# Kernel optimization log

Measured on AMD Instinct MI355X. Metric: run time of the kernel, lower is better.

The kernel has to match this reference:

```python
import jax, jax.numpy as jnp
import numpy as np

RES = 192
VOXEL_LEN = 2.0 / (RES - 1)
AABB_LO, AABB_HI = -1.0, 1.0
SH_DIM = 9
UNIFORM = 0.5

_C0 = 0.28209479177387814
_C1 = 0.4886025119029199
_C2 = (1.0925484305920792, -1.0925484305920792, 0.31539156525252005,
       -1.0925484305920792, 0.5462742152960396)

_CORNERS = np.array([[-1, -1, -1], [-1, -1, 1], [-1, 1, -1], [-1, 1, 1],
                     [1, -1, -1], [1, -1, 1], [1, 1, -1], [1, 1, 1]], dtype=np.float32)


def _sh_basis(d):
    # degree-2 real spherical harmonics basis, [B, 9]
    x, y, z = d[..., 0], d[..., 1], d[..., 2]
    return jnp.stack([
        jnp.full_like(x, _C0),
        -_C1 * y, _C1 * z, -_C1 * x,
        _C2[0] * x * y, _C2[1] * y * z,
        _C2[2] * (2.0 * z * z - x * x - y * y),
        _C2[3] * x * z, _C2[4] * (x * x - y * y),
    ], axis=-1)


def _interp_weights(xyz):
    # trilinear weights matching get_interp_weights corner ordering, [..., 8]
    x, y, z = xyz[..., 0], xyz[..., 1], xyz[..., 2]
    return jnp.stack([
        (1 - x) * (1 - y) * (1 - z), (1 - x) * (1 - y) * z,
        (1 - x) * y * (1 - z), (1 - x) * y * z,
        x * (1 - y) * (1 - z), x * (1 - y) * z,
        x * y * (1 - z), x * y * z], axis=-1)


def setup_inputs() -> dict:
    key = jax.random.key(0)
    k1, k2, k3 = jax.random.split(key, 3)
    B = 1024
    # rays originating on a radius-3 sphere, pointing roughly at the aabb center
    rays_o = jax.random.normal(k1, (B, 3), dtype=jnp.float32)
    rays_o = 3.0 * rays_o / jnp.linalg.norm(rays_o, axis=-1, keepdims=True)
    rays_d = -rays_o / 3.0 + 0.08 * jax.random.normal(k2, (B, 3), dtype=jnp.float32)
    rays_d = rays_d / jnp.linalg.norm(rays_d, axis=-1, keepdims=True)
    grid_data = 0.1 * jax.random.normal(k3, (RES ** 3, 3 * SH_DIM + 1), dtype=jnp.float32)
    grid_idx = jnp.arange(RES ** 3, dtype=jnp.int32).reshape(RES, RES, RES)
    return {"rays_o": rays_o, "rays_d": rays_d, "grid_data": grid_data,
            "grid_idx": grid_idx, "n_samples": 400}


def reference(rays_o, rays_d, grid_data, grid_idx, n_samples):
    B = rays_o.shape[0]
    step = VOXEL_LEN
    # --- get_intersections (no-grad in original) ---
    op = (AABB_HI - rays_o) / rays_d
    on = (AABB_LO - rays_o) / rays_d
    t_in = jnp.max(jnp.minimum(op, on), axis=-1)   # [B]
    t_out = jnp.min(jnp.maximum(op, on), axis=-1)  # [B]
    w = jnp.linspace(0.0, 1.0, n_samples, dtype=rays_o.dtype)
    start = t_in + UNIFORM * step
    end = t_in + UNIFORM * step * n_samples
    intrs = start[:, None] * (1.0 - w) + end[:, None] * w   # [B, S]
    intrs = jax.lax.stop_gradient(jnp.minimum(intrs, t_out[:, None]))

    # --- get_intersection_ids: neighbor voxel gather coordinates ---
    pts = rays_o[:, None, :] + intrs[:, :, None] * rays_d[:, None, :]  # [B,S,3]
    offs = jnp.asarray(_CORNERS) * (VOXEL_LEN / 2)                      # [8,3]
    neigh = pts[:, :, None, :] + offs[None, None]                       # [B,S,8,3]
    ngc = jnp.floor(neigh / VOXEL_LEN + 1e-5)
    centers = jnp.clip((ngc + 0.5) * VOXEL_LEN,
                       AABB_LO + VOXEL_LEN / 2, AABB_HI - VOXEL_LEN / 2)
    ids = jnp.clip((ngc + RES / 2).astype(jnp.int32), 0, RES - 1)
    xyzs = (pts - centers[:, :, 0, :]) / VOXEL_LEN                      # [B,S,3]
    nidx = grid_idx[ids[..., 0], ids[..., 1], ids[..., 2]]              # [B,S,8]

    # --- gather + trilinear interpolation (weights are non-diff in original) ---
    nd = grid_data[nidx]                                                 # [B,S,8,28]
    weights = jax.lax.stop_gradient(_interp_weights(xyzs))              # [B,S,8]
    feat = jnp.einsum('bsec,bse->bsc', nd, weights)                      # [B,S,28]

    sigma = feat[..., -1]                                                # [B,S]
    sh = feat[..., :-1].reshape(B, -1, 3, SH_DIM)                        # [B,S,3,9]
    dirs = rays_d / jnp.linalg.norm(rays_d, axis=-1, keepdims=True)
    rgb = jnp.einsum('bsck,bk->bsc', sh, _sh_basis(dirs))                # [B,S,3]

    # --- volumetric_rendering (uses S-1 intervals) ---
    dists = jnp.diff(intrs, axis=1) * jnp.linalg.norm(rays_d, axis=-1, keepdims=True)
    alpha = 1.0 - jnp.exp(-jax.nn.relu(sigma[:, :-1]) * dists)           # [B,S-1]
    cum = jnp.concatenate([jnp.ones((B, 1), alpha.dtype),
                           jnp.cumprod(1.0 - alpha[:, :-1] + 1e-10, axis=-1)], axis=-1)
    abs_light = alpha * cum
    acc = abs_light.sum(-1)
    rgb_map = (abs_light[..., None] * jax.nn.sigmoid(rgb[:, :-1])).sum(axis=1)  # [B,3]
    depth = jax.lax.stop_gradient((abs_light * intrs[:, :-1]).sum(-1))
    rgb_map = rgb_map + (1.0 - acc[:, None])  # white background
    return rgb_map, alpha, depth
```

## Files before the change

kernel.cpp:

```cpp
#include <hip/hip_runtime.h>
#include <cstddef>


constexpr int   RES  = 192;
constexpr float VLEN = 2.0f / 191.0f;
constexpr int   SM1  = 399;

__global__ __launch_bounds__(512) void nerf_render(
    const float* __restrict__ rays_o,
    const float* __restrict__ rays_d,
    const float* __restrict__ grid_data,
    float* __restrict__ out, int B)
{
  const int b    = blockIdx.x;
  const int tid  = threadIdx.x;
  const int wave = tid >> 6;
  const int lane = tid & 63;
  const int srel = lane >> 3;
  const int r    = lane & 7;

  __shared__ float s_alpha[SM1];
  __shared__ float s_rgb0[SM1];
  __shared__ float s_rgb1[SM1];
  __shared__ float s_rgb2[SM1];
  __shared__ float s_bs[9];

  const float ox = rays_o[b*3+0], oy = rays_o[b*3+1], oz = rays_o[b*3+2];
  const float dx = rays_d[b*3+0], dy = rays_d[b*3+1], dz = rays_d[b*3+2];

  const float opx = (1.0f - ox)/dx, onx = (-1.0f - ox)/dx;
  const float opy = (1.0f - oy)/dy, ony = (-1.0f - oy)/dy;
  const float opz = (1.0f - oz)/dz, onz = (-1.0f - oz)/dz;
  const float t_in  = fmaxf(fmaxf(fminf(opx,onx), fminf(opy,ony)), fminf(opz,onz));
  const float t_out = fminf(fminf(fmaxf(opx,onx), fmaxf(opy,ony)), fmaxf(opz,onz));
  const float h = 0.5f * VLEN;
  const float dnorm = sqrtf(dx*dx + dy*dy + dz*dz);

  {
    const float inv = 1.0f / dnorm;
    const float x = dx*inv, y = dy*inv, z = dz*inv;
    if (tid == 0) {
      s_bs[0] = 0.28209479177387814f;
      s_bs[1] = -0.4886025119029199f * y;
      s_bs[2] =  0.4886025119029199f * z;
      s_bs[3] = -0.4886025119029199f * x;
      s_bs[4] =  1.0925484305920792f * x*y;
      s_bs[5] = -1.0925484305920792f * y*z;
      s_bs[6] =  0.31539156525252005f * (2.0f*z*z - x*x - y*y);
      s_bs[7] = -1.0925484305920792f * x*z;
      s_bs[8] =  0.5462742152960396f * (x*x - y*y);
    }
  }
  __syncthreads();

  float c0[4], c1[4], c2[4], cs[4];
  #pragma unroll
  for (int j = 0; j < 4; ++j) {
    const int c = 4*r + j;
    float b0 = 0.0f, b1 = 0.0f, b2 = 0.0f, bsg = 0.0f;
    if (c < 9)       b0  = s_bs[c];
    else if (c < 18) b1  = s_bs[c - 9];
    else if (c < 27) b2  = s_bs[c - 18];
    else if (c == 27) bsg = 1.0f;
    c0[j] = b0; c1[j] = b1; c2[j] = b2; cs[j] = bsg;
  }

  float* out_rgb   = out;
  float* out_alpha = out + (size_t)B*3;
  float* out_depth = out + (size_t)B*3 + (size_t)B*SM1;

  const float hv = 0.5f * VLEN;
  const float inv_vlen = 1.0f / VLEN;

  #pragma unroll
  for (int p = 0; p < 7; ++p) {
    const int s = p*64 + wave*8 + srel;
    if (s < SM1) {
      const float t  = fminf(t_in + h*(float)(s+1), t_out);
      const float tn = fminf(t_in + h*(float)(s+2), t_out);
      const float px = ox + t*dx, py = oy + t*dy, pz = oz + t*dz;

      const float nx0 = floorf((px - hv)*inv_vlen + 1e-5f);
      const float nx1 = floorf((px + hv)*inv_vlen + 1e-5f);
      const float ny0 = floorf((py - hv)*inv_vlen + 1e-5f);
      const float ny1 = floorf((py + hv)*inv_vlen + 1e-5f);
      const float nz0 = floorf((pz - hv)*inv_vlen + 1e-5f);
      const float nz1 = floorf((pz + hv)*inv_vlen + 1e-5f);

      const int ix0 = min(max((int)(nx0 + 96.0f), 0), RES-1);
      const int ix1 = min(max((int)(nx1 + 96.0f), 0), RES-1);
      const int iy0 = min(max((int)(ny0 + 96.0f), 0), RES-1);
      const int iy1 = min(max((int)(ny1 + 96.0f), 0), RES-1);
      const int iz0 = min(max((int)(nz0 + 96.0f), 0), RES-1);
      const int iz1 = min(max((int)(nz1 + 96.0f), 0), RES-1);

      const float cx = fminf(fmaxf((nx0 + 0.5f)*VLEN, -1.0f + hv), 1.0f - hv);
      const float cy = fminf(fmaxf((ny0 + 0.5f)*VLEN, -1.0f + hv), 1.0f - hv);
      const float cz = fminf(fmaxf((nz0 + 0.5f)*VLEN, -1.0f + hv), 1.0f - hv);
      const float fx = (px - cx)*inv_vlen, fy = (py - cy)*inv_vlen, fz = (pz - cz)*inv_vlen;

      const int xo0 = ix0 * (RES*RES*28), xo1 = ix1 * (RES*RES*28);
      const int yo0 = iy0 * (RES*28),     yo1 = iy1 * (RES*28);
      const int zo0 = iz0 * 28,           zo1 = iz1 * 28;
      const float wx0 = 1.0f - fx, wx1 = fx;
      const float wy0 = 1.0f - fy, wy1 = fy;
      const float wz0 = 1.0f - fz, wz1 = fz;

      int   offs[8];
      float w[8];
      #pragma unroll
      for (int e = 0; e < 8; ++e) {
        offs[e] = ((e & 4) ? xo1 : xo0) + ((e & 2) ? yo1 : yo0) + ((e & 1) ? zo1 : zo0);
        w[e]    = ((e & 4) ? wx1 : wx0) * ((e & 2) ? wy1 : wy0) * ((e & 1) ? wz1 : wz0);
      }

      float4 v[8];
      #pragma unroll
      for (int e = 0; e < 8; ++e) v[e] = make_float4(0.f, 0.f, 0.f, 0.f);
      if (r < 7) {
        #pragma unroll
        for (int e = 0; e < 8; ++e)
          v[e] = *reinterpret_cast<const float4*>(grid_data + offs[e] + 4*r);
      }

      float4 a = make_float4(0.f, 0.f, 0.f, 0.f);
      #pragma unroll
      for (int e = 0; e < 8; ++e) {
        a.x = fmaf(w[e], v[e].x, a.x);
        a.y = fmaf(w[e], v[e].y, a.y);
        a.z = fmaf(w[e], v[e].z, a.z);
        a.w = fmaf(w[e], v[e].w, a.w);
      }

      float pr0 = a.x*c0[0] + a.y*c0[1] + a.z*c0[2] + a.w*c0[3];
      float pr1 = a.x*c1[0] + a.y*c1[1] + a.z*c1[2] + a.w*c1[3];
      float pr2 = a.x*c2[0] + a.y*c2[1] + a.z*c2[2] + a.w*c2[3];
      float sg  = a.x*cs[0] + a.y*cs[1] + a.z*cs[2] + a.w*cs[3];

      #pragma unroll
      for (int o = 1; o <= 4; o <<= 1) {
        pr0 += __shfl_xor(pr0, o, 64);
        pr1 += __shfl_xor(pr1, o, 64);
        pr2 += __shfl_xor(pr2, o, 64);
        sg  += __shfl_xor(sg,  o, 64);
      }

      if (r == 0) {
        const float dist = (tn - t) * dnorm;
        const float sig  = fmaxf(sg, 0.0f);
        const float al   = 1.0f - __expf(-sig * dist);
        s_alpha[s] = al;
        out_alpha[(size_t)b*SM1 + s] = al;
        s_rgb0[s] = 1.0f/(1.0f + __expf(-pr0));
        s_rgb1[s] = 1.0f/(1.0f + __expf(-pr1));
        s_rgb2[s] = 1.0f/(1.0f + __expf(-pr2));
      }
    }
  }
  __syncthreads();

  if (tid < 64) {
    const int ln = tid;
    const int s0 = ln * 7;
    float pr = 1.0f;
    #pragma unroll
    for (int i = 0; i < 7; ++i) {
      const int si = s0 + i;
      const float tt = (si < SM1) ? (1.0f - s_alpha[si] + 1e-10f) : 1.0f;
      pr *= tt;
    }
    float incl = pr;
    #pragma unroll
    for (int off = 1; off < 64; off <<= 1) {
      const float vv = __shfl_up(incl, off, 64);
      if (ln >= off) incl *= vv;
    }
    float cum = __shfl_up(incl, 1, 64);
    if (ln == 0) cum = 1.0f;

    float acc = 0.0f, r0 = 0.0f, r1 = 0.0f, r2 = 0.0f, dep = 0.0f;
    #pragma unroll
    for (int i = 0; i < 7; ++i) {
      const int si = s0 + i;
      if (si < SM1) {
        const float al = s_alpha[si];
        const float ab = al * cum;
        acc += ab;
        r0 = fmaf(ab, s_rgb0[si], r0);
        r1 = fmaf(ab, s_rgb1[si], r1);
        r2 = fmaf(ab, s_rgb2[si], r2);
        const float ti = fminf(t_in + h*(float)(si+1), t_out);
        dep = fmaf(ab, ti, dep);
        cum *= (1.0f - al + 1e-10f);
      }
    }
    #pragma unroll
    for (int off = 32; off; off >>= 1) {
      acc += __shfl_down(acc, off, 64);
      r0  += __shfl_down(r0,  off, 64);
      r1  += __shfl_down(r1,  off, 64);
      r2  += __shfl_down(r2,  off, 64);
      dep += __shfl_down(dep, off, 64);
    }
    if (ln == 0) {
      const float bg = 1.0f - acc;
      out_rgb[b*3+0] = r0 + bg;
      out_rgb[b*3+1] = r1 + bg;
      out_rgb[b*3+2] = r2 + bg;
      out_depth[b]   = dep;
    }
  }
}

extern "C" void kernel_launch(void* const* d_in, const int* in_sizes, int n_in,
                              void* d_out, int out_size, void* d_ws, size_t ws_size,
                              hipStream_t stream) {
  const float* rays_o    = (const float*)d_in[0];
  const float* rays_d    = (const float*)d_in[1];
  const float* grid_data = (const float*)d_in[2];
  const int B = in_sizes[0] / 3;
  nerf_render<<<dim3(B), dim3(512), 0, stream>>>(
      rays_o, rays_d, grid_data, (float*)d_out, B);
}
```

Before: 33.04 us.

## Precompute sample geometry in shared memory and double-buffer voxel gathers

Each thread now computes the voxel offsets and fractional weights for one sample up front and stores them in shared memory. Previously all 8 lanes of a sample group recomputed the same geometry. The gather loop is software-pipelined: the eight float4 voxel loads for the next pass are issued before the current pass is reduced, to hide global-memory latency. Alpha output is written coalesced after the loop instead of by scattered r==0 lanes. The cost is more shared memory and roughly double the vector registers held for the in-flight loads, which may reduce occupancy.

```diff
diff --git a/kernel.cpp b/kernel.cpp
--- a/kernel.cpp
+++ b/kernel.cpp
@@ -5,6 +5,7 @@
 constexpr int   RES  = 192;
 constexpr float VLEN = 2.0f / 191.0f;
 constexpr int   SM1  = 399;
+constexpr int   ROWB = 28 * 4;
 
 __global__ __launch_bounds__(512) void nerf_render(
     const float* __restrict__ rays_o,
@@ -23,6 +24,9 @@
   __shared__ float s_rgb0[SM1];
   __shared__ float s_rgb1[SM1];
   __shared__ float s_rgb2[SM1];
+  __shared__ int4  s_m0[SM1];
+  __shared__ int4  s_m1[SM1];
+  __shared__ float s_m2[SM1];
   __shared__ float s_bs[9];
 
   const float ox = rays_o[b*3+0], oy = rays_o[b*3+1], oz = rays_o[b*3+2];
@@ -36,20 +40,53 @@
   const float h = 0.5f * VLEN;
   const float dnorm = sqrtf(dx*dx + dy*dy + dz*dz);
 
-  {
+  if (tid == 0) {
     const float inv = 1.0f / dnorm;
     const float x = dx*inv, y = dy*inv, z = dz*inv;
-    if (tid == 0) {
-      s_bs[0] = 0.28209479177387814f;
-      s_bs[1] = -0.4886025119029199f * y;
-      s_bs[2] =  0.4886025119029199f * z;
-      s_bs[3] = -0.4886025119029199f * x;
-      s_bs[4] =  1.0925484305920792f * x*y;
-      s_bs[5] = -1.0925484305920792f * y*z;
-      s_bs[6] =  0.31539156525252005f * (2.0f*z*z - x*x - y*y);
-      s_bs[7] = -1.0925484305920792f * x*z;
-      s_bs[8] =  0.5462742152960396f * (x*x - y*y);
-    }
+    s_bs[0] = 0.28209479177387814f;
+    s_bs[1] = -0.4886025119029199f * y;
+    s_bs[2] =  0.4886025119029199f * z;
+    s_bs[3] = -0.4886025119029199f * x;
+    s_bs[4] =  1.0925484305920792f * x*y;
+    s_bs[5] = -1.0925484305920792f * y*z;
+    s_bs[6] =  0.31539156525252005f * (2.0f*z*z - x*x - y*y);
+    s_bs[7] = -1.0925484305920792f * x*z;
+    s_bs[8] =  0.5462742152960396f * (x*x - y*y);
+  }
+
+  const float hv = 0.5f * VLEN;
+  const float inv_vlen = 1.0f / VLEN;
+
+  if (tid < SM1) {
+    const int s = tid;
+    const float t  = fminf(t_in + h*(float)(s+1), t_out);
+    const float px = ox + t*dx, py = oy + t*dy, pz = oz + t*dz;
+
+    const float nx0 = floorf((px - hv)*inv_vlen + 1e-5f);
+    const float nx1 = floorf((px + hv)*inv_vlen + 1e-5f);
+    const float ny0 = floorf((py - hv)*inv_vlen + 1e-5f);
+    const float ny1 = floorf((py + hv)*inv_vlen + 1e-5f);
+    const float nz0 = floorf((pz - hv)*inv_vlen + 1e-5f);
+    const float nz1 = floorf((pz + hv)*inv_vlen + 1e-5f);
+
+    const int ix0 = min(max((int)(nx0 + 96.0f), 0), RES-1);
+    const int ix1 = min(max((int)(nx1 + 96.0f), 0), RES-1);
+    const int iy0 = min(max((int)(ny0 + 96.0f), 0), RES-1);
+    const int iy1 = min(max((int)(ny1 + 96.0f), 0), RES-1);
+    const int iz0 = min(max((int)(nz0 + 96.0f), 0), RES-1);
+    const int iz1 = min(max((int)(nz1 + 96.0f), 0), RES-1);
+
+    const float cx = fminf(fmaxf((nx0 + 0.5f)*VLEN, -1.0f + hv), 1.0f - hv);
+    const float cy = fminf(fmaxf((ny0 + 0.5f)*VLEN, -1.0f + hv), 1.0f - hv);
+    const float cz = fminf(fmaxf((nz0 + 0.5f)*VLEN, -1.0f + hv), 1.0f - hv);
+    const float fx = (px - cx)*inv_vlen, fy = (py - cy)*inv_vlen, fz = (pz - cz)*inv_vlen;
+
+    const int x0 = ix0 * (RES*RES*ROWB), x1 = ix1 * (RES*RES*ROWB);
+    const int y0 = iy0 * (RES*ROWB),     y1 = iy1 * (RES*ROWB);
+    s_m0[s] = make_int4(x0 + y0, x0 + y1, x1 + y0, x1 + y1);
+    s_m1[s] = make_int4(iz0 * ROWB, iz1 * ROWB,
+                        __float_as_int(fx), __float_as_int(fy));
+    s_m2[s] = fz;
   }
   __syncthreads();
 
@@ -69,95 +106,78 @@
   float* out_alpha = out + (size_t)B*3;
   float* out_depth = out + (size_t)B*3 + (size_t)B*SM1;
 
-  const float hv = 0.5f * VLEN;
-  const float inv_vlen = 1.0f / VLEN;
-
+  const char* gbase = (const char*)grid_data + 16*min(r, 6);
+
+  float4 va[2][8];
+  int4   m1s[2];
+  float  m2s[2];
+
+  auto issue = [&](int p, int slot) {
+    const int sc = min(p*64 + wave*8 + srel, SM1-1);
+    const int4 a0 = s_m0[sc];
+    const int4 a1 = s_m1[sc];
+    m1s[slot] = a1;
+    m2s[slot] = s_m2[sc];
+    va[slot][0] = *reinterpret_cast<const float4*>(gbase + (a0.x + a1.x));
+    va[slot][1] = *reinterpret_cast<const float4*>(gbase + (a0.x + a1.y));
+    va[slot][2] = *reinterpret_cast<const float4*>(gbase + (a0.y + a1.x));
+    va[slot][3] = *reinterpret_cast<const float4*>(gbase + (a0.y + a1.y));
+    va[slot][4] = *reinterpret_cast<const float4*>(gbase + (a0.z + a1.x));
+    va[slot][5] = *reinterpret_cast<const float4*>(gbase + (a0.z + a1.y));
+    va[slot][6] = *reinterpret_cast<const float4*>(gbase + (a0.w + a1.x));
+    va[slot][7] = *reinterpret_cast<const float4*>(gbase + (a0.w + a1.y));
+  };
+
+  auto consume = [&](int p, int slot) {
+    const int s = p*64 + wave*8 + srel;
+    if (s >= SM1) return;
+    const float fx = __int_as_float(m1s[slot].z);
+    const float fy = __int_as_float(m1s[slot].w);
+    const float fz = m2s[slot];
+    const float wx0 = 1.0f - fx, wy0 = 1.0f - fy, wz0 = 1.0f - fz;
+    const float p00 = wx0*wy0, p01 = wx0*fy, p10 = fx*wy0, p11 = fx*fy;
+    const float w[8] = { p00*wz0, p00*fz, p01*wz0, p01*fz,
+                         p10*wz0, p10*fz, p11*wz0, p11*fz };
+    float ax = 0.f, ay = 0.f, az = 0.f, aw = 0.f;
+    #pragma unroll
+    for (int e = 0; e < 8; ++e) {
+      ax = fmaf(w[e], va[slot][e].x, ax);
+      ay = fmaf(w[e], va[slot][e].y, ay);
+      az = fmaf(w[e], va[slot][e].z, az);
+      aw = fmaf(w[e], va[slot][e].w, aw);
+    }
+    float pr0 = ax*c0[0] + ay*c0[1] + az*c0[2] + aw*c0[3];
+    float pr1 = ax*c1[0] + ay*c1[1] + az*c1[2] + aw*c1[3];
+    float pr2 = ax*c2[0] + ay*c2[1] + az*c2[2] + aw*c2[3];
+    float sg  = ax*cs[0] + ay*cs[1] + az*cs[2] + aw*cs[3];
+    #pragma unroll
+    for (int o = 1; o <= 4; o <<= 1) {
+      pr0 += __shfl_xor(pr0, o, 64);
+      pr1 += __shfl_xor(pr1, o, 64);
+      pr2 += __shfl_xor(pr2, o, 64);
+      sg  += __shfl_xor(sg,  o, 64);
+    }
+    if (r == 0) {
+      const float t  = fminf(t_in + h*(float)(s+1), t_out);
+      const float tn = fminf(t_in + h*(float)(s+2), t_out);
+      const float dist = (tn - t) * dnorm;
+      const float sig  = fmaxf(sg, 0.0f);
+      s_alpha[s] = 1.0f - __expf(-sig * dist);
+      s_rgb0[s] = 1.0f/(1.0f + __expf(-pr0));
+      s_rgb1[s] = 1.0f/(1.0f + __expf(-pr1));
+      s_rgb2[s] = 1.0f/(1.0f + __expf(-pr2));
+    }
+  };
+
+  issue(0, 0);
   #pragma unroll
   for (int p = 0; p < 7; ++p) {
-    const int s = p*64 + wave*8 + srel;
-    if (s < SM1) {
-      const float t  = fminf(t_in + h*(float)(s+1), t_out);
-      const float tn = fminf(t_in + h*(float)(s+2), t_out);
-      const float px = ox + t*dx, py = oy + t*dy, pz = oz + t*dz;
-
-      const float nx0 = floorf((px - hv)*inv_vlen + 1e-5f);
-      const float nx1 = floorf((px + hv)*inv_vlen + 1e-5f);
-      const float ny0 = floorf((py - hv)*inv_vlen + 1e-5f);
-      const float ny1 = floorf((py + hv)*inv_vlen + 1e-5f);
-      const float nz0 = floorf((pz - hv)*inv_vlen + 1e-5f);
-      const float nz1 = floorf((pz + hv)*inv_vlen + 1e-5f);
-
-      const int ix0 = min(max((int)(nx0 + 96.0f), 0), RES-1);
-      const int ix1 = min(max((int)(nx1 + 96.0f), 0), RES-1);
-      const int iy0 = min(max((int)(ny0 + 96.0f), 0), RES-1);
-      const int iy1 = min(max((int)(ny1 + 96.0f), 0), RES-1);
-      const int iz0 = min(max((int)(nz0 + 96.0f), 0), RES-1);
-      const int iz1 = min(max((int)(nz1 + 96.0f), 0), RES-1);
-
-      const float cx = fminf(fmaxf((nx0 + 0.5f)*VLEN, -1.0f + hv), 1.0f - hv);
-      const float cy = fminf(fmaxf((ny0 + 0.5f)*VLEN, -1.0f + hv), 1.0f - hv);
-      const float cz = fminf(fmaxf((nz0 + 0.5f)*VLEN, -1.0f + hv), 1.0f - hv);
-      const float fx = (px - cx)*inv_vlen, fy = (py - cy)*inv_vlen, fz = (pz - cz)*inv_vlen;
-
-      const int xo0 = ix0 * (RES*RES*28), xo1 = ix1 * (RES*RES*28);
-      const int yo0 = iy0 * (RES*28),     yo1 = iy1 * (RES*28);
-      const int zo0 = iz0 * 28,           zo1 = iz1 * 28;
-      const float wx0 = 1.0f - fx, wx1 = fx;
-      const float wy0 = 1.0f - fy, wy1 = fy;
-      const float wz0 = 1.0f - fz, wz1 = fz;
-
-      int   offs[8];
-      float w[8];
-      #pragma unroll
-      for (int e = 0; e < 8; ++e) {
-        offs[e] = ((e & 4) ? xo1 : xo0) + ((e & 2) ? yo1 : yo0) + ((e & 1) ? zo1 : zo0);
-        w[e]    = ((e & 4) ? wx1 : wx0) * ((e & 2) ? wy1 : wy0) * ((e & 1) ? wz1 : wz0);
-      }
-
-      float4 v[8];
-      #pragma unroll
-      for (int e = 0; e < 8; ++e) v[e] = make_float4(0.f, 0.f, 0.f, 0.f);
-      if (r < 7) {
-        #pragma unroll
-        for (int e = 0; e < 8; ++e)
-          v[e] = *reinterpret_cast<const float4*>(grid_data + offs[e] + 4*r);
-      }
-
-      float4 a = make_float4(0.f, 0.f, 0.f, 0.f);
-      #pragma unroll
-      for (int e = 0; e < 8; ++e) {
-        a.x = fmaf(w[e], v[e].x, a.x);
-        a.y = fmaf(w[e], v[e].y, a.y);
-        a.z = fmaf(w[e], v[e].z, a.z);
-        a.w = fmaf(w[e], v[e].w, a.w);
-      }
-
-      float pr0 = a.x*c0[0] + a.y*c0[1] + a.z*c0[2] + a.w*c0[3];
-      float pr1 = a.x*c1[0] + a.y*c1[1] + a.z*c1[2] + a.w*c1[3];
-      float pr2 = a.x*c2[0] + a.y*c2[1] + a.z*c2[2] + a.w*c2[3];
-      float sg  = a.x*cs[0] + a.y*cs[1] + a.z*cs[2] + a.w*cs[3];
-
-      #pragma unroll
-      for (int o = 1; o <= 4; o <<= 1) {
-        pr0 += __shfl_xor(pr0, o, 64);
-        pr1 += __shfl_xor(pr1, o, 64);
-        pr2 += __shfl_xor(pr2, o, 64);
-        sg  += __shfl_xor(sg,  o, 64);
-      }
-
-      if (r == 0) {
-        const float dist = (tn - t) * dnorm;
-        const float sig  = fmaxf(sg, 0.0f);
-        const float al   = 1.0f - __expf(-sig * dist);
-        s_alpha[s] = al;
-        out_alpha[(size_t)b*SM1 + s] = al;
-        s_rgb0[s] = 1.0f/(1.0f + __expf(-pr0));
-        s_rgb1[s] = 1.0f/(1.0f + __expf(-pr1));
-        s_rgb2[s] = 1.0f/(1.0f + __expf(-pr2));
-      }
-    }
+    if (p < 6) issue(p + 1, (p + 1) & 1);
+    consume(p, p & 1);
   }
   __syncthreads();
+
+  if (tid < SM1) out_alpha[(size_t)b*SM1 + tid] = s_alpha[tid];
 
   if (tid < 64) {
     const int ln = tid;
```

Measured after the change: 33.72 us. 2.0% more time.
